# Optimization experiments

Measured on AMD Instinct MI355X. Metric: run time of the kernel, lower is better.

## Reference

```python
import jax, jax.numpy as jnp
import numpy as np

SEQ, SUB, B, V = 32, 16, 512, 258
U = SEQ // SUB
Z, CH, CO, DH = 512, 1024, 512, 1024


def _lstm_cell(x, h, c, Wi, Wh, bi, bh):
    # torch gate order: input, forget, cell, output
    g = x @ Wi + h @ Wh + bi + bh  # [B, 4H]
    i, f, gg, o = jnp.split(g, 4, axis=-1)
    c = jax.nn.sigmoid(f) * c + jax.nn.sigmoid(i) * jnp.tanh(gg)
    h = jax.nn.sigmoid(o) * jnp.tanh(c)
    return h, c


def _lstm2(xs, h1_0, p1, p2):
    # xs: [T,B,in]; h1_0: [B,H] layer-1 initial hidden.
    # Layer-2 hidden and both cell states start at zero (initialize_state in torch code).
    z0 = jnp.zeros_like(h1_0)
    def step(carry, x):
        h1, c1, h2, c2 = carry
        h1, c1 = _lstm_cell(x, h1, c1, *p1)
        h2, c2 = _lstm_cell(h1, h2, c2, *p2)
        return (h1, c1, h2, c2), h2
    _, hs = jax.lax.scan(step, (h1_0, z0, z0, z0), xs)
    return hs  # [T,B,H] top-layer hidden states


def setup_inputs() -> dict:
    key = jax.random.key(0)
    ks = iter(jax.random.split(key, 40))
    def w(shape, s=0.05):
        return jax.random.normal(next(ks), shape, dtype=jnp.float32) * s
    return {
        "z": jax.random.normal(next(ks), (B, Z), dtype=jnp.float32),
        "x": jax.random.uniform(next(ks), (SEQ, B, V), dtype=jnp.float32),
        "conductor_input": w((1, B, V)),
        "ci_W": w((Z, CH)), "ci_b": w((CH,)),
        "cW1i": w((V, 4 * CH)), "cW1h": w((CH, 4 * CH)), "cb1i": w((4 * CH,)), "cb1h": w((4 * CH,)),
        "cW2i": w((CH, 4 * CH)), "cW2h": w((CH, 4 * CH)), "cb2i": w((4 * CH,)), "cb2h": w((4 * CH,)),
        "co_W": w((CH, CO)), "co_b": w((CO,)),
        "di_W": w((CO, DH)), "di_b": w((DH,)),
        "dW1i": w((CO + V, 4 * DH)), "dW1h": w((DH, 4 * DH)), "db1i": w((4 * DH,)), "db1h": w((4 * DH,)),
        "dW2i": w((DH, 4 * DH)), "dW2h": w((DH, 4 * DH)), "db2i": w((4 * DH,)), "db2h": w((4 * DH,)),
        "fc_W": w((DH, V)), "fc_b": w((V,)),
    }


def reference(z, x, conductor_input, ci_W, ci_b, cW1i, cW1h, cb1i, cb1h, cW2i, cW2h, cb2i, cb2h, co_W, co_b, di_W, di_b, dW1i, dW1h, db1i, db1h, dW2i, dW2h, db2i, db2h, fc_W, fc_b):
    # --- conductor: 2-layer LSTM over U steps of a learned constant input ---
    h1 = jnp.tanh(z @ ci_W + ci_b)  # [B,CH] layer-1 init hidden
    cin = jnp.broadcast_to(conductor_input, (U, B, V))
    ch = _lstm2(cin, h1, (cW1i, cW1h, cb1i, cb1h), (cW2i, cW2h, cb2i, cb2h))  # [U,B,CH]
    c = ch @ co_W + co_b  # [U,B,CO]
    # --- decoder (teacher forcing): state resets each sub-sequence, so the U
    # segments of length SUB are independent given c -> vmap over segments ---
    sos = jnp.zeros((1, B, V), jnp.float32).at[:, :, 0].set(1.0)
    prev = jnp.concatenate([sos, x[:-1]], axis=0).reshape(U, SUB, B, V)
    cb = jnp.broadcast_to(c[:, None], (U, SUB, B, CO))
    dec_in = jnp.concatenate([cb, prev], axis=-1)  # [U,SUB,B,CO+V]
    def run_seg(xs, cj):
        h1_0 = jnp.tanh(cj @ di_W + di_b)  # [B,DH]
        return _lstm2(xs, h1_0, (dW1i, dW1h, db1i, db1h), (dW2i, dW2h, db2i, db2h))
    hs = jax.vmap(run_seg)(dec_in, c)  # [U,SUB,B,DH]
    logp = jax.nn.log_softmax(hs @ fc_W + fc_b, axis=-1)  # log(softmax(.)) fused
    return logp.reshape(SEQ, B, V).transpose(1, 0, 2)  # [B,SEQ,V]
```

## Files before the change

kernel.cpp:

```cpp
#include <hip/hip_runtime.h>
#include <cstddef>
#include <cstdint>


namespace {

typedef short s8v __attribute__((ext_vector_type(8)));
typedef float f4v __attribute__((ext_vector_type(4)));
typedef unsigned short ushort_t;

__device__ inline unsigned short f2bf(float f) {
    union { float f; unsigned u; } v; v.f = f;
    unsigned r = v.u + 0x7fff + ((v.u >> 16) & 1);
    return (unsigned short)(r >> 16);
}
__device__ inline float bf2f(ushort_t u) {
    union { unsigned u; float f; } v; v.u = ((unsigned)u) << 16; return v.f;
}
__device__ inline float sigm_f(float x) { return 1.f / (1.f + __expf(-x)); }
__device__ inline float tanh_f(float x) {
    const float e = __expf(2.f * fabsf(x));
    return copysignf(1.f - 2.f / (e + 1.f), x);
}

#define GLOAD_LDS(gp, lp)                                              \
    __builtin_amdgcn_global_load_lds(                                  \
        (const __attribute__((address_space(1))) void*)(gp),           \
        (__attribute__((address_space(3))) void*)(lp), 16, 0, 0)

__device__ __forceinline__ void gemm_core(
    const ushort_t* __restrict__ A1a, const ushort_t* __restrict__ A1b,
    int lda1, int K1, const ushort_t* __restrict__ W1,
    const ushort_t* __restrict__ A2, int lda2, int K2,
    const ushort_t* __restrict__ W2,
    int bm, int bn, ushort_t* lds, f4v acc[4][4])
{
    const int tid = threadIdx.x;
    const int wid = tid >> 6;
    const int lane = tid & 63;
    const int wr = wid >> 2;
    const int wc = wid & 3;
    const int lrow = lane & 15, lkg = lane >> 4;

    const int n1 = K1 >> 5;
    const int n2 = (W2 != nullptr) ? (K2 >> 5) : 0;
    const int nt = n1 + n2;

    const int srow = wid * 16 + (lane >> 2);
    const int ssrc = (((lane & 3) ^ ((srow >> 1) & 3)) << 3);

    auto arow = [&](const ushort_t* Aa, const ushort_t* Ab, int lda,
                    int r) -> const ushort_t* {
        return (Ab != nullptr && r >= 512) ? Ab + (size_t)(r - 512) * lda
                                           : Aa + (size_t)r * lda;
    };
    const ushort_t* pA1 = arow(A1a, A1b, lda1, bm + srow) + ssrc;
    const ushort_t* pA2 = nullptr;
    if (n2 > 0) pA2 = A2 + (size_t)(bm + srow) * lda2 + ssrc;

    auto stageA = [&](int idx, int buf) {
        const ushort_t* p;
        if (idx < n1) p = pA1 + (idx << 5);
        else          p = pA2 + ((idx - n1) << 5);
        GLOAD_LDS(p, lds + buf * 4096 + wid * 512);
    };

    const int nb0 = (bn >> 4) + wc * 4;
    const ushort_t* W1l = W1 + (size_t)nb0 * n1 * 512 + lane * 8;
    const ushort_t* W2l = (n2 > 0) ? (W2 + (size_t)nb0 * n2 * 512 + lane * 8) : nullptr;

    auto loadB = [&](int t, s8v (&b)[4]) {
        const ushort_t* base; int kb, KB;
        if (t < n1) { base = W1l; kb = t; KB = n1; }
        else        { base = W2l; kb = t - n1; KB = n2; }
#pragma unroll
        for (int n = 0; n < 4; ++n)
            b[n] = *(const s8v*)(base + ((size_t)(n * KB + kb) << 9));
    };

    int aoff[4];
#pragma unroll
    for (int m = 0; m < 4; ++m) {
        const int r = wr * 64 + m * 16 + lrow;
        aoff[m] = r * 32 + ((lkg ^ ((r >> 1) & 3)) << 3);
    }

    s8v b0[4], b1[4];
    loadB(0, b0);
    stageA(0, 0);
    loadB(1, b1);
    stageA(1, 1);

    int cbuf = 0, sbuf = 2;
    auto iter = [&](int t, s8v (&bcur)[4]) {
        if (t + 1 < nt) asm volatile("s_waitcnt vmcnt(5)" ::: "memory");
        else            asm volatile("s_waitcnt vmcnt(0)" ::: "memory");
        __builtin_amdgcn_s_barrier();
        __builtin_amdgcn_sched_barrier(0);
        if (t + 2 < nt) {
            stageA(t + 2, sbuf);
            sbuf = (sbuf == 2) ? 0 : sbuf + 1;
        }
        const ushort_t* L = lds + cbuf * 4096;
        s8v a[4];
#pragma unroll
        for (int m = 0; m < 4; ++m) a[m] = *(const s8v*)(L + aoff[m]);
        __builtin_amdgcn_s_setprio(1);
#pragma unroll
        for (int m = 0; m < 4; ++m)
#pragma unroll
            for (int n = 0; n < 4; ++n)
                acc[m][n] = __builtin_amdgcn_mfma_f32_16x16x32_bf16(
                    a[m], bcur[n], acc[m][n], 0, 0, 0);
        __builtin_amdgcn_s_setprio(0);
        if (t + 2 < nt) loadB(t + 2, bcur);
        cbuf = (cbuf == 2) ? 0 : cbuf + 1;
    };

    int t = 0;
    while (true) {
        iter(t, b0); if (++t == nt) break;
        iter(t, b1); if (++t == nt) break;
    }
}

template <int ACT>
__global__ __launch_bounds__(512, 2) void plain_gemm(
    const ushort_t* __restrict__ A, int lda, int K,
    const ushort_t* __restrict__ W,
    const float* __restrict__ bias, int bias_n,
    float* __restrict__ C, ushort_t* __restrict__ Cbf, int N)
{
    __shared__ __align__(16) ushort_t lds[3 * 4096];
    const int bm = blockIdx.x * 128, bn = blockIdx.y * 256;
    f4v acc[4][4] = {};
    gemm_core(A, nullptr, lda, K, W, nullptr, 0, 0, nullptr, bm, bn, lds, acc);

    const int tid = threadIdx.x, wid = tid >> 6, lane = tid & 63;
    const int wr = wid >> 2, wc = wid & 3, lrow = lane & 15, lkg = lane >> 4;
#pragma unroll
    for (int m = 0; m < 4; ++m) {
        const int row0 = bm + wr * 64 + m * 16 + lkg * 4;
#pragma unroll
        for (int n = 0; n < 4; ++n) {
            const int col = bn + wc * 64 + n * 16 + lrow;
            const float bv = (bias != nullptr && col < bias_n) ? bias[col] : 0.f;
#pragma unroll
            for (int r = 0; r < 4; ++r) {
                float v = acc[m][n][r] + bv;
                if (ACT == 1) v = tanh_f(v);
                const size_t o = (size_t)(row0 + r) * N + col;
                if (C != nullptr) C[o] = v;
                if (Cbf != nullptr) Cbf[o] = f2bf(v);
            }
        }
    }
}

struct Prob {
    const ushort_t* A1a; const ushort_t* A1b; int lda1; int K1;
    const ushort_t* B1t;
    const ushort_t* A2; int lda2; int K2; const ushort_t* B2t;
    const ushort_t* Dbf;
    const float* bias;
    float* cst;
    ushort_t* hout;
    ushort_t* hs;
    int step_s;
};

__global__ __launch_bounds__(512, 2) void lstm_step(Prob PA, int nxa, Prob PB,
                                                    int mshift)
{
    __shared__ __align__(16) ushort_t lds[3 * 4096];
    const int nblk = gridDim.x;
    const int wg = blockIdx.x;
    const int swz = (wg & 7) * (nblk >> 3) + (wg >> 3);
    const int nmb = 1 << mshift;
    const int nb = swz >> mshift;
    const int mb = swz & (nmb - 1);

    const bool isA = mb < nxa;
    const Prob& P = isA ? PA : PB;
    const int bm = (isA ? mb : mb - nxa) * 128;
    const int bn = nb * 256;

    f4v acc[4][4] = {};
    gemm_core(P.A1a, P.A1b, P.lda1, P.K1, P.B1t,
              P.A2, P.lda2, P.K2, P.B2t, bm, bn, lds, acc);

    const int tid = threadIdx.x, wid = tid >> 6, lane = tid & 63;
    const int wr = wid >> 2, wc = wid & 3, lrow = lane & 15, lkg = lane >> 4;
    const int colbase = bn + wc * 64;
    const int jb = (colbase >> 6) * 16 + lrow;

#pragma unroll
    for (int m = 0; m < 4; ++m) {
        const int row0 = bm + wr * 64 + m * 16 + lkg * 4;
#pragma unroll
        for (int r = 0; r < 4; ++r) {
            const int row = row0 + r;
            float g0 = acc[m][0][r], g1 = acc[m][1][r];
            float g2 = acc[m][2][r], g3 = acc[m][3][r];
            if (P.Dbf != nullptr) {
                const ushort_t* d = P.Dbf + (size_t)row * 4096 + colbase + lrow;
                g0 += bf2f(d[0]); g1 += bf2f(d[16]);
                g2 += bf2f(d[32]); g3 += bf2f(d[48]);
            }
            if (P.bias != nullptr) {
                const float* b = P.bias + colbase + lrow;
                g0 += b[0]; g1 += b[16]; g2 += b[32]; g3 += b[48];
            }
            const size_t ci = (size_t)row * 1024 + jb;
            const float cn = fmaf(sigm_f(g1), P.cst[ci], sigm_f(g0) * tanh_f(g2));
            const float hn = sigm_f(g3) * tanh_f(cn);
            P.cst[ci] = cn;
            const ushort_t hb = f2bf(hn);
            P.hout[ci] = hb;
            if (P.hs != nullptr) {
                size_t d;
                if (P.step_s >= 0) {
                    const int u = row >> 9, b = row & 511;
                    d = ((size_t)((u * 16 + P.step_s) * 512 + b) << 10) + jb;
                } else {
                    d = ci;
                }
                P.hs[d] = hb;
            }
        }
    }
}

template <int PERM>
__global__ __launch_bounds__(256) void pack_frag_bf16(
    const float* __restrict__ in, ushort_t* __restrict__ out,
    int K, int N, int Kp, int Np)
{
    __shared__ float tile[32][33];
    const int kb = blockIdx.x;
    const int np0 = blockIdx.y * 32;
    const int k0 = kb * 32;
    const int tx = threadIdx.x & 31;
    const int ty = threadIdx.x >> 5;
#pragma unroll
    for (int q = 0; q < 4; ++q) {
        const int k = k0 + ty + 8 * q;
        const int np = np0 + tx;
        int n;
        if (PERM) n = ((np >> 4) & 3) * 1024 + (np >> 6) * 16 + (np & 15);
        else      n = np;
        tile[ty + 8 * q][tx] = (k < K && n < N) ? in[(size_t)k * N + n] : 0.f;
    }
    __syncthreads();
    const int t = threadIdx.x;
    const int rec = t >> 7;
    const int lane = (t >> 1) & 63;
    const int half = t & 1;
    const size_t grec = (size_t)(np0 / 16 + rec) * (Kp / 32) + kb;
    const int kl = (lane >> 4) * 8 + half * 4;
    const int nl = rec * 16 + (lane & 15);
    ushort4 v;
    v.x = f2bf(tile[kl + 0][nl]);
    v.y = f2bf(tile[kl + 1][nl]);
    v.z = f2bf(tile[kl + 2][nl]);
    v.w = f2bf(tile[kl + 3][nl]);
    *(ushort4*)(out + (grec * 64 + lane) * 8 + half * 4) = v;
}

__global__ void convert_pad_bf16(const float* __restrict__ in,
                                 ushort_t* __restrict__ out,
                                 int K, int Kp, int total)
{
    const int idx = blockIdx.x * 256 + threadIdx.x;
    if (idx >= total) return;
    const int r = idx / Kp, k = idx - r * Kp;
    out[idx] = (k < K) ? f2bf(in[(size_t)r * K + k]) : (ushort_t)0;
}

__global__ void sos_init_bf16(ushort_t* __restrict__ sos)
{
    const int i = blockIdx.x * 256 + threadIdx.x;
    if (i < 512 * 320) sos[i] = ((i % 320) == 0) ? (ushort_t)0x3F80 : (ushort_t)0;
}

__global__ void permute_bias(const float* __restrict__ b1,
                             const float* __restrict__ b2,
                             float* __restrict__ out)
{
    const int c = blockIdx.x * 256 + threadIdx.x;
    if (c >= 4096) return;
    const int g = (c >> 4) & 3;
    const int j = (c >> 6) * 16 + (c & 15);
    out[c] = b1[g * 1024 + j] + b2[g * 1024 + j];
}

__global__ __launch_bounds__(256) void logsoftmax_kernel(
    const float* __restrict__ logits, float* __restrict__ out)
{
    const int row = blockIdx.x;
    const int tid = threadIdx.x;
    const float* L = logits + (size_t)row * 512;
    const int t = row >> 9;
    const int b = row & 511;
    float* O = out + ((size_t)b * 32 + t) * 258;

    const float x0 = L[tid];
    const float x1 = (tid < 2) ? L[256 + tid] : -1e30f;

    __shared__ float sm[4];
    float m = fmaxf(x0, x1);
#pragma unroll
    for (int off = 32; off > 0; off >>= 1) m = fmaxf(m, __shfl_down(m, off));
    if ((tid & 63) == 0) sm[tid >> 6] = m;
    __syncthreads();
    m = fmaxf(fmaxf(sm[0], sm[1]), fmaxf(sm[2], sm[3]));
    __syncthreads();

    float s = expf(x0 - m) + ((tid < 2) ? expf(x1 - m) : 0.f);
#pragma unroll
    for (int off = 32; off > 0; off >>= 1) s += __shfl_down(s, off);
    if ((tid & 63) == 0) sm[tid >> 6] = s;
    __syncthreads();
    s = sm[0] + sm[1] + sm[2] + sm[3];

    const float lse = m + logf(s);
    O[tid] = x0 - lse;
    if (tid < 2) O[256 + tid] = x1 - lse;
}

}

extern "C" void kernel_launch(void* const* d_in, const int* in_sizes, int n_in,
                              void* d_out, int out_size, void* d_ws, size_t ws_size,
                              hipStream_t stream)
{
    (void)in_sizes; (void)n_in; (void)out_size; (void)ws_size;

    const float* z    = (const float*)d_in[0];
    const float* x    = (const float*)d_in[1];
    const float* cin  = (const float*)d_in[2];
    const float* ciW  = (const float*)d_in[3];
    const float* cib  = (const float*)d_in[4];
    const float* cW1i = (const float*)d_in[5];
    const float* cW1h = (const float*)d_in[6];
    const float* cb1i = (const float*)d_in[7];
    const float* cb1h = (const float*)d_in[8];
    const float* cW2i = (const float*)d_in[9];
    const float* cW2h = (const float*)d_in[10];
    const float* cb2i = (const float*)d_in[11];
    const float* cb2h = (const float*)d_in[12];
    const float* coW  = (const float*)d_in[13];
    const float* cob  = (const float*)d_in[14];
    const float* diW  = (const float*)d_in[15];
    const float* dib  = (const float*)d_in[16];
    const float* dW1i = (const float*)d_in[17];
    const float* dW1h = (const float*)d_in[18];
    const float* db1i = (const float*)d_in[19];
    const float* db1h = (const float*)d_in[20];
    const float* dW2i = (const float*)d_in[21];
    const float* dW2h = (const float*)d_in[22];
    const float* db2i = (const float*)d_in[23];
    const float* db2h = (const float*)d_in[24];
    const float* fcW  = (const float*)d_in[25];
    const float* fcb  = (const float*)d_in[26];
    float* out = (float*)d_out;

    char* wsp = (char*)d_ws;
    size_t off = 0;
    auto allocf = [&](size_t n) { float* p = (float*)(wsp + off); off += n * 4; return p; };
    auto allocb = [&](size_t n) { ushort_t* p = (ushort_t*)(wsp + off); off += n * 2; return p; };

    float* cst = allocf((size_t)3 * 1024 * 1024 + 64);
    float* c1c = cst;
    float* c2c = cst + (size_t)512 * 1024;
    float* c1d = cst + (size_t)1024 * 1024;
    float* c2d = cst + (size_t)2 * 1024 * 1024;
    float* pb1c = allocf(4096);
    float* pb2c = allocf(4096);
    float* pb1d = allocf(4096);
    float* pb2d = allocf(4096);
    float* logits = allocf((size_t)16384 * 512);

    ushort_t* h2z  = allocb((size_t)2 * (512 + 1024) * 1024);
    ushort_t* hc2A = h2z;
    ushort_t* hc2B = h2z + (size_t)512 * 1024;
    ushort_t* h2dA = h2z + (size_t)2 * 512 * 1024;
    ushort_t* h2dB = h2z + (size_t)(2 * 512 + 1024) * 1024;

    ushort_t* hc1A = allocb((size_t)512 * 1024);
    ushort_t* hc1B = allocb((size_t)512 * 1024);
    ushort_t* h1dA = allocb((size_t)1024 * 1024);
    ushort_t* h1dB = allocb((size_t)1024 * 1024);

    ushort_t* zbf    = allocb((size_t)512 * 512);
    ushort_t* cinbf  = allocb((size_t)512 * 320);
    ushort_t* sosbf  = allocb((size_t)512 * 320);
    ushort_t* xbf    = allocb((size_t)16384 * 320);
    ushort_t* chbf   = allocb((size_t)1024 * 1024);
    ushort_t* ccode  = allocb((size_t)1024 * 512);
    ushort_t* cpre   = allocb((size_t)1024 * 4096);
    ushort_t* xW1c   = allocb((size_t)512 * 4096);
    ushort_t* hsbf   = allocb((size_t)16384 * 1024);

    ushort_t* ciWp  = allocb((size_t)1024 * 512);
    ushort_t* cW1ip = allocb((size_t)4096 * 320);
    ushort_t* cW1hp = allocb((size_t)4096 * 1024);
    ushort_t* cW2ip = allocb((size_t)4096 * 1024);
    ushort_t* cW2hp = allocb((size_t)4096 * 1024);
    ushort_t* coWp  = allocb((size_t)512 * 1024);
    ushort_t* dtopp = allocb((size_t)4096 * 512);
    ushort_t* dbotp = allocb((size_t)4096 * 320);
    ushort_t* diWp  = allocb((size_t)1024 * 512);
    ushort_t* dW1hp = allocb((size_t)4096 * 1024);
    ushort_t* dW2ip = allocb((size_t)4096 * 1024);
    ushort_t* dW2hp = allocb((size_t)4096 * 1024);
    ushort_t* fcWp  = allocb((size_t)512 * 1024);

    hipMemsetAsync(cst, 0, (size_t)3 * 1024 * 1024 * 4, stream);
    hipMemsetAsync(h2z, 0, (size_t)2 * (512 + 1024) * 1024 * 2, stream);

    auto pack = [&](const float* in, ushort_t* o, int K, int N, int Kp, int Np, int perm) {
        dim3 g(Kp / 32, Np / 32);
        if (perm) pack_frag_bf16<1><<<g, 256, 0, stream>>>(in, o, K, N, Kp, Np);
        else      pack_frag_bf16<0><<<g, 256, 0, stream>>>(in, o, K, N, Kp, Np);
    };
    pack(ciW, ciWp, 512, 1024, 512, 1024, 0);
    pack(cW1i, cW1ip, 258, 4096, 320, 4096, 1);
    pack(cW1h, cW1hp, 1024, 4096, 1024, 4096, 1);
    pack(cW2i, cW2ip, 1024, 4096, 1024, 4096, 1);
    pack(cW2h, cW2hp, 1024, 4096, 1024, 4096, 1);
    pack(coW, coWp, 1024, 512, 1024, 512, 0);
    pack(dW1i, dtopp, 512, 4096, 512, 4096, 1);
    pack(dW1i + (size_t)512 * 4096, dbotp, 258, 4096, 320, 4096, 1);
    pack(diW, diWp, 512, 1024, 512, 1024, 0);
    pack(dW1h, dW1hp, 1024, 4096, 1024, 4096, 1);
    pack(dW2i, dW2ip, 1024, 4096, 1024, 4096, 1);
    pack(dW2h, dW2hp, 1024, 4096, 1024, 4096, 1);
    pack(fcW, fcWp, 1024, 258, 1024, 512, 0);

    auto convert = [&](const float* in, ushort_t* o, int K, int Kp, int R) {
        const int total = R * Kp;
        convert_pad_bf16<<<dim3((total + 255) / 256), 256, 0, stream>>>(in, o, K, Kp, total);
    };
    convert(z, zbf, 512, 512, 512);
    convert(cin, cinbf, 258, 320, 512);
    convert(x, xbf, 258, 320, 16384);
    sos_init_bf16<<<dim3((512 * 320 + 255) / 256), 256, 0, stream>>>(sosbf);
    permute_bias<<<16, 256, 0, stream>>>(cb1i, cb1h, pb1c);
    permute_bias<<<16, 256, 0, stream>>>(cb2i, cb2h, pb2c);
    permute_bias<<<16, 256, 0, stream>>>(db1i, db1h, pb1d);
    permute_bias<<<16, 256, 0, stream>>>(db2i, db2h, pb2d);

    auto gemm = [&](int act, const ushort_t* A, int lda, int K, const ushort_t* W,
                    const float* bias, int bias_n,
                    float* C, ushort_t* Cbf, int M, int N) {
        dim3 g(M / 128, N / 256);
        if (act) plain_gemm<1><<<g, 512, 0, stream>>>(A, lda, K, W, bias, bias_n, C, Cbf, N);
        else     plain_gemm<0><<<g, 512, 0, stream>>>(A, lda, K, W, bias, bias_n, C, Cbf, N);
    };

    gemm(1, zbf, 512, 512, ciWp, cib, 1024, nullptr, hc1A, 512, 1024);
    gemm(0, cinbf, 320, 320, cW1ip, pb1c, 4096, nullptr, xW1c, 512, 4096);

    ushort_t* HC1[2] = {hc1A, hc1B};
    ushort_t* HC2[2] = {hc2A, hc2B};
    for (int k = 0; k <= 2; ++k) {
        Prob pa{}, pb{};
        int nxa = 0, nxb = 0;
        if (k < 2) {
            pa = {HC1[k & 1], nullptr, 1024, 1024, cW1hp,
                  nullptr, 0, 0, nullptr,
                  xW1c, nullptr, c1c, HC1[(k + 1) & 1], nullptr, -1};
            nxa = 4;
        }
        if (k >= 1) {
            pb = {HC1[k & 1], nullptr, 1024, 1024, cW2ip,
                  HC2[k & 1], 1024, 1024, cW2hp,
                  nullptr, pb2c, c2c, HC2[(k + 1) & 1],
                  chbf + (size_t)(k - 1) * 512 * 1024, -1};
            nxb = 4;
        }
        const int nmb = nxa + nxb;
        const int mshift = (nmb == 4) ? 2 : 3;
        lstm_step<<<dim3(nmb * 16), 512, 0, stream>>>(pa, nxa, pb, mshift);
    }

    gemm(0, chbf, 1024, 1024, coWp, cob, 512, nullptr, ccode, 1024, 512);
    gemm(0, ccode, 512, 512, dtopp, pb1d, 4096, nullptr, cpre, 1024, 4096);
    gemm(1, ccode, 512, 512, diWp, dib, 1024, nullptr, h1dA, 1024, 1024);

    ushort_t* H1[2] = {h1dA, h1dB};
    ushort_t* H2[2] = {h2dA, h2dB};
    for (int k = 0; k <= 16; ++k) {
        Prob pa{}, pb{};
        int nxa = 0, nxb = 0;
        if (k < 16) {
            const ushort_t* plo = (k == 0) ? sosbf : (xbf + (size_t)(k - 1) * 512 * 320);
            const ushort_t* phi = xbf + (size_t)(15 + k) * 512 * 320;
            pa = {plo, phi, 320, 320, dbotp,
                  H1[k & 1], 1024, 1024, dW1hp,
                  cpre, nullptr, c1d, H1[(k + 1) & 1], nullptr, -1};
            nxa = 8;
        }
        if (k >= 1) {
            pb = {H1[k & 1], nullptr, 1024, 1024, dW2ip,
                  H2[k & 1], 1024, 1024, dW2hp,
                  nullptr, pb2d, c2d, H2[(k + 1) & 1], hsbf, k - 1};
            nxb = 8;
        }
        const int nmb = nxa + nxb;
        const int mshift = (nmb == 8) ? 3 : 4;
        lstm_step<<<dim3(nmb * 16), 512, 0, stream>>>(pa, nxa, pb, mshift);
    }

    gemm(0, hsbf, 1024, 1024, fcWp, fcb, 258, logits, nullptr, 16384, 512);
    logsoftmax_kernel<<<dim3(16384), 256, 0, stream>>>(logits, out);
}
```

Baseline: 1.285 ms.

## Rewrite LSTM step as LDS-free per-wave GEMM on fragment-packed operands

The recurrent LSTM step kernel drops the shared-memory gemm_core and has each wave compute a 64x64 tile. It loads A and B operands straight from global memory, which are pre-laid out in MFMA fragment order with double-buffered registers. Hidden states and the x/sos inputs are now written and packed in that fragment layout, so every lane issues one contiguous 16-byte load per fragment. The goal is to remove LDS staging and barrier cost and give the small-M recurrent GEMMs more parallel waves. The trade-off is less operand reuse across waves and more global/L2 traffic per FLOP.

```diff
diff --git a/kernel.cpp b/kernel.cpp
--- a/kernel.cpp
+++ b/kernel.cpp
@@ -21,6 +21,12 @@
 __device__ inline float tanh_f(float x) {
     const float e = __expf(2.f * fabsf(x));
     return copysignf(1.f - 2.f / (e + 1.f), x);
+}
+
+__device__ inline size_t fragA_addr(int row, int col, int KB) {
+    const size_t rec = (size_t)(row >> 4) * KB + (col >> 5);
+    const int l = (row & 15) + (((col >> 3) & 3) << 4);
+    return (rec << 9) + (l << 3) + (col & 7);
 }
 
 #define GLOAD_LDS(gp, lp)                                              \
@@ -38,8 +44,7 @@
     const int tid = threadIdx.x;
     const int wid = tid >> 6;
     const int lane = tid & 63;
-    const int wr = wid >> 2;
-    const int wc = wid & 3;
+    const int wr = wid >> 2, wc = wid & 3;
     const int lrow = lane & 15, lkg = lane >> 4;
 
     const int n1 = K1 >> 5;
@@ -129,7 +134,7 @@
     const ushort_t* __restrict__ A, int lda, int K,
     const ushort_t* __restrict__ W,
     const float* __restrict__ bias, int bias_n,
-    float* __restrict__ C, ushort_t* __restrict__ Cbf, int N)
+    float* __restrict__ C, ushort_t* __restrict__ Cbf, int cbf_frag, int N)
 {
     __shared__ __align__(16) ushort_t lds[3 * 4096];
     const int bm = blockIdx.x * 128, bn = blockIdx.y * 256;
@@ -149,18 +154,24 @@
             for (int r = 0; r < 4; ++r) {
                 float v = acc[m][n][r] + bv;
                 if (ACT == 1) v = tanh_f(v);
-                const size_t o = (size_t)(row0 + r) * N + col;
-                if (C != nullptr) C[o] = v;
-                if (Cbf != nullptr) Cbf[o] = f2bf(v);
+                const int row = row0 + r;
+                if (C != nullptr) C[(size_t)row * N + col] = v;
+                if (Cbf != nullptr) {
+                    const size_t o = cbf_frag ? fragA_addr(row, col, 32)
+                                              : (size_t)row * N + col;
+                    Cbf[o] = f2bf(v);
+                }
             }
         }
     }
 }
 
-struct Prob {
-    const ushort_t* A1a; const ushort_t* A1b; int lda1; int K1;
-    const ushort_t* B1t;
-    const ushort_t* A2; int lda2; int K2; const ushort_t* B2t;
+struct ProbW {
+    const ushort_t* A1;
+    const ushort_t* A1b;
+    int K1;
+    const ushort_t* W1;
+    const ushort_t* A2; int K2; const ushort_t* W2;
     const ushort_t* Dbf;
     const float* bias;
     float* cst;
@@ -169,59 +180,121 @@
     int step_s;
 };
 
-__global__ __launch_bounds__(512, 2) void lstm_step(Prob PA, int nxa, Prob PB,
-                                                    int mshift)
-{
-    __shared__ __align__(16) ushort_t lds[3 * 4096];
+__global__ __launch_bounds__(256, 2) void lstm_step(ProbW PA, int nxa,
+                                                    ProbW PB, int nmshift)
+{
+    const int tid = threadIdx.x;
+    const int wid = tid >> 6, lane = tid & 63;
     const int nblk = gridDim.x;
-    const int wg = blockIdx.x;
-    const int swz = (wg & 7) * (nblk >> 3) + (wg >> 3);
-    const int nmb = 1 << mshift;
-    const int nb = swz >> mshift;
-    const int mb = swz & (nmb - 1);
-
-    const bool isA = mb < nxa;
-    const Prob& P = isA ? PA : PB;
-    const int bm = (isA ? mb : mb - nxa) * 128;
-    const int bn = nb * 256;
+    const int b = blockIdx.x;
+    const int swzb = (b & 7) * (nblk >> 3) + (b >> 3);
+    const int wt = swzb * 4 + wid;
+    const int nm = 1 << nmshift;
+    const int nbw = wt >> nmshift;
+    const int mbw = wt & (nm - 1);
+
+    const bool isA = mbw < nxa;
+    const ProbW& P = isA ? PA : PB;
+    const int mb64 = isA ? mbw : mbw - nxa;
+    const int lrow = lane & 15, lkg = lane >> 4;
+
+    const int KB1 = P.K1 >> 5;
+    const int KB2 = (P.W2 != nullptr) ? (P.K2 >> 5) : 0;
+    const int nt = KB1 + KB2;
+    const int mbrec0 = mb64 * 4;
+    const int nb0 = nbw * 4;
+
+    const ushort_t* A1sel =
+        (P.A1b != nullptr && mbrec0 >= 32)
+            ? P.A1b + (((size_t)(mbrec0 - 32) * KB1) << 9) + lane * 8
+            : P.A1 + (((size_t)mbrec0 * KB1) << 9) + lane * 8;
+    const ushort_t* A2sel =
+        (KB2 > 0) ? P.A2 + (((size_t)mbrec0 * KB2) << 9) + lane * 8 : nullptr;
+    const ushort_t* W1l = P.W1 + (((size_t)nb0 * KB1) << 9) + lane * 8;
+    const ushort_t* W2l =
+        (KB2 > 0) ? P.W2 + (((size_t)nb0 * KB2) << 9) + lane * 8 : nullptr;
+
+    auto loadA = [&](int t, s8v (&a)[4]) {
+        if (t < KB1) {
+#pragma unroll
+            for (int m = 0; m < 4; ++m)
+                a[m] = *(const s8v*)(A1sel + ((size_t)(m * KB1 + t) << 9));
+        } else {
+            const int t2 = t - KB1;
+#pragma unroll
+            for (int m = 0; m < 4; ++m)
+                a[m] = *(const s8v*)(A2sel + ((size_t)(m * KB2 + t2) << 9));
+        }
+    };
+    auto loadB = [&](int t, s8v (&bb)[4]) {
+        if (t < KB1) {
+#pragma unroll
+            for (int n = 0; n < 4; ++n)
+                bb[n] = *(const s8v*)(W1l + ((size_t)(n * KB1 + t) << 9));
+        } else {
+            const int t2 = t - KB1;
+#pragma unroll
+            for (int n = 0; n < 4; ++n)
+                bb[n] = *(const s8v*)(W2l + ((size_t)(n * KB2 + t2) << 9));
+        }
+    };
 
     f4v acc[4][4] = {};
-    gemm_core(P.A1a, P.A1b, P.lda1, P.K1, P.B1t,
-              P.A2, P.lda2, P.K2, P.B2t, bm, bn, lds, acc);
-
-    const int tid = threadIdx.x, wid = tid >> 6, lane = tid & 63;
-    const int wr = wid >> 2, wc = wid & 3, lrow = lane & 15, lkg = lane >> 4;
-    const int colbase = bn + wc * 64;
-    const int jb = (colbase >> 6) * 16 + lrow;
-
+    s8v a0[4], b0[4], a1[4], b1[4];
+    loadA(0, a0); loadB(0, b0);
+    loadA(1, a1); loadB(1, b1);
+
+    auto mm = [&](s8v (&a)[4], s8v (&bb)[4]) {
+        __builtin_amdgcn_s_setprio(1);
+#pragma unroll
+        for (int m = 0; m < 4; ++m)
+#pragma unroll
+            for (int n = 0; n < 4; ++n)
+                acc[m][n] = __builtin_amdgcn_mfma_f32_16x16x32_bf16(
+                    a[m], bb[n], acc[m][n], 0, 0, 0);
+        __builtin_amdgcn_s_setprio(0);
+    };
+
+    int t = 0;
+    while (true) {
+        mm(a0, b0);
+        if (t + 2 < nt) { loadA(t + 2, a0); loadB(t + 2, b0); }
+        if (++t == nt) break;
+        mm(a1, b1);
+        if (t + 2 < nt) { loadA(t + 2, a1); loadB(t + 2, b1); }
+        if (++t == nt) break;
+    }
+
+    const int bm = mb64 * 64, bn = nbw * 64;
+    const int jb = (bn >> 6) * 16 + lrow;
 #pragma unroll
     for (int m = 0; m < 4; ++m) {
-        const int row0 = bm + wr * 64 + m * 16 + lkg * 4;
+        const int row0 = bm + m * 16 + lkg * 4;
 #pragma unroll
         for (int r = 0; r < 4; ++r) {
             const int row = row0 + r;
             float g0 = acc[m][0][r], g1 = acc[m][1][r];
             float g2 = acc[m][2][r], g3 = acc[m][3][r];
             if (P.Dbf != nullptr) {
-                const ushort_t* d = P.Dbf + (size_t)row * 4096 + colbase + lrow;
+                const ushort_t* d = P.Dbf + (size_t)row * 4096 + bn + lrow;
                 g0 += bf2f(d[0]); g1 += bf2f(d[16]);
                 g2 += bf2f(d[32]); g3 += bf2f(d[48]);
             }
             if (P.bias != nullptr) {
-                const float* b = P.bias + colbase + lrow;
-                g0 += b[0]; g1 += b[16]; g2 += b[32]; g3 += b[48];
+                const float* bb = P.bias + bn + lrow;
+                g0 += bb[0]; g1 += bb[16]; g2 += bb[32]; g3 += bb[48];
             }
             const size_t ci = (size_t)row * 1024 + jb;
             const float cn = fmaf(sigm_f(g1), P.cst[ci], sigm_f(g0) * tanh_f(g2));
             const float hn = sigm_f(g3) * tanh_f(cn);
             P.cst[ci] = cn;
             const ushort_t hb = f2bf(hn);
-            P.hout[ci] = hb;
+            P.hout[fragA_addr(row, jb, 32)] = hb;
             if (P.hs != nullptr) {
                 size_t d;
                 if (P.step_s >= 0) {
-                    const int u = row >> 9, b = row & 511;
-                    d = ((size_t)((u * 16 + P.step_s) * 512 + b) << 10) + jb;
+                    const int u = row >> 9, bq = row & 511;
+                    d = ((size_t)((u * 16 + P.step_s) * 512 + bq) << 10) + jb;
                 } else {
                     d = ci;
                 }
@@ -267,6 +340,40 @@
     *(ushort4*)(out + (grec * 64 + lane) * 8 + half * 4) = v;
 }
 
+__global__ void pack_fragA(const float* __restrict__ in,
+                           ushort_t* __restrict__ out, int M, int K, int KB,
+                           int total)
+{
+    const int idx = blockIdx.x * 256 + threadIdx.x;
+    if (idx >= total) return;
+    const int lane = idx & 63;
+    const int rec = idx >> 6;
+    const int kb = rec % KB, mb = rec / KB;
+    const int row = mb * 16 + (lane & 15);
+    const int k0 = kb * 32 + (lane >> 4) * 8;
+    ushort_t v[8];
+#pragma unroll
+    for (int j = 0; j < 8; ++j) {
+        const int k = k0 + j;
+        v[j] = (k < K) ? f2bf(in[(size_t)row * K + k]) : (ushort_t)0;
+    }
+    *(s8v*)(out + ((size_t)idx << 3)) = *(const s8v*)v;
+}
+
+__global__ void sos_pack(ushort_t* __restrict__ out)
+{
+    const int idx = blockIdx.x * 256 + threadIdx.x;
+    if (idx >= 32 * 10 * 64) return;
+    const int lane = idx & 63;
+    const int rec = idx >> 6;
+    const int kb = rec % 10;
+    const int k0 = kb * 32 + (lane >> 4) * 8;
+    ushort_t v[8];
+#pragma unroll
+    for (int j = 0; j < 8; ++j) v[j] = (k0 + j == 0) ? (ushort_t)0x3F80 : (ushort_t)0;
+    *(s8v*)(out + ((size_t)idx << 3)) = *(const s8v*)v;
+}
+
 __global__ void convert_pad_bf16(const float* __restrict__ in,
                                  ushort_t* __restrict__ out,
                                  int K, int Kp, int total)
@@ -275,12 +382,6 @@
     if (idx >= total) return;
     const int r = idx / Kp, k = idx - r * Kp;
     out[idx] = (k < K) ? f2bf(in[(size_t)r * K + k]) : (ushort_t)0;
-}
-
-__global__ void sos_init_bf16(ushort_t* __restrict__ sos)
-{
-    const int i = blockIdx.x * 256 + threadIdx.x;
-    if (i < 512 * 320) sos[i] = ((i % 320) == 0) ? (ushort_t)0x3F80 : (ushort_t)0;
 }
 
 __global__ void permute_bias(const float* __restrict__ b1,
@@ -394,13 +495,13 @@
 
     ushort_t* zbf    = allocb((size_t)512 * 512);
     ushort_t* cinbf  = allocb((size_t)512 * 320);
-    ushort_t* sosbf  = allocb((size_t)512 * 320);
-    ushort_t* xbf    = allocb((size_t)16384 * 320);
     ushort_t* chbf   = allocb((size_t)1024 * 1024);
     ushort_t* ccode  = allocb((size_t)1024 * 512);
     ushort_t* cpre   = allocb((size_t)1024 * 4096);
     ushort_t* xW1c   = allocb((size_t)512 * 4096);
     ushort_t* hsbf   = allocb((size_t)16384 * 1024);
+    ushort_t* xpk    = allocb((size_t)1024 * 10 * 512);
+    ushort_t* sospk  = allocb((size_t)32 * 10 * 512);
 
     ushort_t* ciWp  = allocb((size_t)1024 * 512);
     ushort_t* cW1ip = allocb((size_t)4096 * 320);
@@ -444,8 +545,11 @@
     };
     convert(z, zbf, 512, 512, 512);
     convert(cin, cinbf, 258, 320, 512);
-    convert(x, xbf, 258, 320, 16384);
-    sos_init_bf16<<<dim3((512 * 320 + 255) / 256), 256, 0, stream>>>(sosbf);
+    {
+        const int total = 1024 * 10 * 64;
+        pack_fragA<<<dim3((total + 255) / 256), 256, 0, stream>>>(x, xpk, 16384, 258, 10, total);
+        sos_pack<<<dim3((32 * 10 * 64 + 255) / 256), 256, 0, stream>>>(sospk);
+    }
     permute_bias<<<16, 256, 0, stream>>>(cb1i, cb1h, pb1c);
     permute_bias<<<16, 256, 0, stream>>>(cb2i, cb2h, pb2c);
     permute_bias<<<16, 256, 0, stream>>>(db1i, db1h, pb1d);
@@ -453,66 +557,69 @@
 
     auto gemm = [&](int act, const ushort_t* A, int lda, int K, const ushort_t* W,
                     const float* bias, int bias_n,
-                    float* C, ushort_t* Cbf, int M, int N) {
+                    float* C, ushort_t* Cbf, int cbf_frag, int M, int N) {
         dim3 g(M / 128, N / 256);
-        if (act) plain_gemm<1><<<g, 512, 0, stream>>>(A, lda, K, W, bias, bias_n, C, Cbf, N);
-        else     plain_gemm<0><<<g, 512, 0, stream>>>(A, lda, K, W, bias, bias_n, C, Cbf, N);
-    };
-
-    gemm(1, zbf, 512, 512, ciWp, cib, 1024, nullptr, hc1A, 512, 1024);
-    gemm(0, cinbf, 320, 320, cW1ip, pb1c, 4096, nullptr, xW1c, 512, 4096);
+        if (act) plain_gemm<1><<<g, 512, 0, stream>>>(A, lda, K, W, bias, bias_n, C, Cbf, cbf_frag, N);
+        else     plain_gemm<0><<<g, 512, 0, stream>>>(A, lda, K, W, bias, bias_n, C, Cbf, cbf_frag, N);
+    };
+
+    gemm(1, zbf, 512, 512, ciWp, cib, 1024, nullptr, hc1A, 1, 512, 1024);
+    gemm(0, cinbf, 320, 320, cW1ip, pb1c, 4096, nullptr, xW1c, 0, 512, 4096);
+
+    auto step = [&](const ProbW& pa, int nxa, const ProbW& pb, int nxb) {
+        const int nm = nxa + nxb;
+        const int nmshift = (nm == 8) ? 3 : (nm == 16) ? 4 : 5;
+        lstm_step<<<dim3(16 * nm), 256, 0, stream>>>(pa, nxa, pb, nmshift);
+    };
 
     ushort_t* HC1[2] = {hc1A, hc1B};
     ushort_t* HC2[2] = {hc2A, hc2B};
     for (int k = 0; k <= 2; ++k) {
-        Prob pa{}, pb{};
+        ProbW pa{}, pb{};
         int nxa = 0, nxb = 0;
         if (k < 2) {
-            pa = {HC1[k & 1], nullptr, 1024, 1024, cW1hp,
-                  nullptr, 0, 0, nullptr,
+            pa = {HC1[k & 1], nullptr, 1024, cW1hp,
+                  nullptr, 0, nullptr,
                   xW1c, nullptr, c1c, HC1[(k + 1) & 1], nullptr, -1};
-            nxa = 4;
+            nxa = 8;
         }
         if (k >= 1) {
-            pb = {HC1[k & 1], nullptr, 1024, 1024, cW2ip,
-                  HC2[k & 1], 1024, 1024, cW2hp,
+            pb = {HC1[k & 1], nullptr, 1024, cW2ip,
+                  HC2[k & 1], 1024, cW2hp,
                   nullptr, pb2c, c2c, HC2[(k + 1) & 1],
                   chbf + (size_t)(k - 1) * 512 * 1024, -1};
-            nxb = 4;
-        }
-        const int nmb = nxa + nxb;
-        const int mshift = (nmb == 4) ? 2 : 3;
-        lstm_step<<<dim3(nmb * 16), 512, 0, stream>>>(pa, nxa, pb, mshift);
-    }
-
-    gemm(0, chbf, 1024, 1024, coWp, cob, 512, nullptr, ccode, 1024, 512);
-    gemm(0, ccode, 512, 512, dtopp, pb1d, 4096, nullptr, cpre, 1024, 4096);
-    gemm(1, ccode, 512, 512, diWp, dib, 1024, nullptr, h1dA, 1024, 1024);
+            nxb = 8;
+        }
+        step(pa, nxa, pb, nxb);
+    }
+
+    gemm(0, chbf, 1024, 1024, coWp, cob, 512, nullptr, ccode, 0, 1024, 512);
+    gemm(0, ccode, 512, 512, dtopp, pb1d, 4096, nullptr, cpre, 0, 1024, 4096);
+    gemm(1, ccode, 512, 512, diWp, dib, 1024, nullptr, h1dA, 1, 1024, 1024);
 
     ushort_t* H1[2] = {h1dA, h1dB};
     ushort_t* H2[2] = {h2dA, h2dB};
+    const size_t SLAB = (size_t)32 * 10 * 512;
     for (int k = 0; k <= 16; ++k) {
-        Prob pa{}, pb{};
+        ProbW pa{}, pb{};
         int nxa = 0, nxb = 0;
         if (k < 16) {
-            const ushort_t* plo = (k == 0) ? sosbf : (xbf + (size_t)(k - 1) * 512 * 320);
-            const ushort_t* phi = xbf + (size_t)(15 + k) * 512 * 320;
-            pa = {plo, phi, 320, 320, dbotp,
-                  H1[k & 1], 1024, 1024, dW1hp,
+            const ushort_t* plo = (k == 0) ? sospk : (xpk + (size_t)(k - 1) * SLAB);
+            const ushort_t* phi = xpk + (size_t)(15 + k) * SLAB;
+            pa = {plo, phi, 320, dbotp,
+                  H1[k & 1], 1024, dW1hp,
                   cpre, nullptr, c1d, H1[(k + 1) & 1], nullptr, -1};
-            nxa = 8;
+            nxa = 16;
         }
         if (k >= 1) {
-            pb = {H1[k & 1], nullptr, 1024, 1024, dW2ip,
-                  H2[k & 1], 1024, 1024, dW2hp,
+            pb = {H1[k & 1], nullptr, 1024, dW2ip,
+                  H2[k & 1], 1024, dW2hp,
                   nullptr, pb2d, c2d, H2[(k + 1) & 1], hsbf, k - 1};
-            nxb = 8;
-        }
-        const int nmb = nxa + nxb;
-        const int mshift = (nmb == 8) ? 3 : 4;
-        lstm_step<<<dim3(nmb * 16), 512, 0, stream>>>(pa, nxa, pb, mshift);
-    }
-
-    gemm(0, hsbf, 1024, 1024, fcWp, fcb, 258, logits, nullptr, 16384, 512);
+            nxb = 16;
+        }
+        step(pa, nxa, pb, nxb);
+    }
+
+    gemm(0, hsbf, 1024, 1024, fcWp, fcb, 258, logits, nullptr, 0, 16384, 512);
     logsoftmax_kernel<<<dim3(16384), 256, 0, stream>>>(logits, out);
 }
```

New measurement: 1.328 ms. 1.03x slower.
